# Performance work log

Measured on AMD Instinct MI355X. Metric: run time of the kernel, lower is better.

The kernel has to match this reference:

```python
import jax, jax.numpy as jnp
import numpy as np

N_USERS, N_ITEMS, D, B = 16384, 4096, 64, 2048
NAN_FRAC = 0.7
EPS = 1e-8


def setup_inputs() -> dict:
    key = jax.random.key(0)
    k1, k2, k3, k4, k5 = jax.random.split(key, 5)
    ratings = jax.random.uniform(k1, (N_USERS, N_ITEMS), jnp.float32, 1.0, 5.0)
    miss = jax.random.uniform(k2, (N_USERS, N_ITEMS)) < NAN_FRAC
    rating_matrix = jnp.where(miss, jnp.nan, ratings)
    user_embeddings = jax.random.normal(k3, (N_USERS, D), jnp.float32)
    user_indices = jax.random.randint(k4, (B,), 0, N_USERS)
    item_indices = jax.random.randint(k5, (B,), 0, N_ITEMS)
    return {
        "rating_matrix": rating_matrix,
        "user_embeddings": user_embeddings,
        "user_indices": user_indices,
        "item_indices": item_indices,
    }


def reference(rating_matrix, user_embeddings, user_indices, item_indices):
    n_users = rating_matrix.shape[0]

    # per-user average over non-NaN ratings (0.0 if user has no ratings)
    valid_r = ~jnp.isnan(rating_matrix)                      # [N, I]
    r0 = jnp.where(valid_r, rating_matrix, 0.0)
    cnt = valid_r.sum(axis=1)
    avg_ratings = jnp.where(cnt > 0, r0.sum(axis=1) / jnp.maximum(cnt, 1), 0.0)  # [N]

    u = user_embeddings[user_indices]                        # [B, d]
    # cosine similarity of each query user vs all users
    dots = jnp.einsum('bd,nd->bn', u, user_embeddings)       # [B, N]
    mag_u = jnp.linalg.norm(u, axis=1, keepdims=True)        # [B, 1]
    mag_v = jnp.linalg.norm(user_embeddings, axis=1)[None]   # [1, N]
    sim = dots / (mag_u * mag_v + EPS)                       # [B, N]

    # ratings of all users on each query item
    ratings_col = rating_matrix[:, item_indices].T           # [B, N]
    mask = ~jnp.isnan(ratings_col)                           # valid neighbor ratings
    mask = mask & (jnp.arange(n_users)[None, :] != user_indices[:, None])  # exclude self

    diff = jnp.where(mask, ratings_col - avg_ratings[None, :], 0.0)
    sim_m = jnp.where(mask, sim, 0.0)
    num = (diff * sim_m).sum(axis=1)                         # [B]
    den = jnp.abs(sim_m).sum(axis=1)                         # [B]
    den_safe = jnp.where(den == 0, 1.0, den)

    avg_u = avg_ratings[user_indices]
    return jnp.where(den == 0, avg_u, avg_u + num / den_safe)
```

## Files before the change

kernel.cpp:

```cpp
#include <hip/hip_runtime.h>
#include <math.h>

#define NU   16384
#define NI   4096
#define DDIM 64
#define BB   2048
#define GSTR8 2056

typedef unsigned short u16;
typedef unsigned char  u8;
typedef __attribute__((ext_vector_type(8))) short short8;
typedef __attribute__((ext_vector_type(4))) float f32x4;

static __device__ __forceinline__ u16 f2bf(float f) {
    union { float f; unsigned int u; } v; v.f = f;
    unsigned int u = v.u + 0x7FFFu + ((v.u >> 16) & 1u);
    return (u16)(u >> 16);
}

static __device__ __forceinline__ u8 enc_r(float r) {
    return (u8)__float2uint_rz(fmaf(r, 50.f, -48.5f));
}

__global__ __launch_bounds__(256) void k_qprep(
    const float* __restrict__ E, const int* __restrict__ uidx,
    u16* __restrict__ Ubf, int2* __restrict__ qinfo)
{
    const int lane = threadIdx.x & 63;
    const int b = blockIdx.x * 4 + (threadIdx.x >> 6);
    const int ub = uidx[b];
    const float e = E[(size_t)ub * DDIM + lane];
    float ss = e * e;
#pragma unroll
    for (int o = 32; o > 0; o >>= 1) ss += __shfl_xor(ss, o);
    Ubf[b * DDIM + lane] = f2bf(e);
    if (lane == 0) qinfo[b] = make_int2(ub, __float_as_int(rsqrtf(ss)));
}

__global__ __launch_bounds__(256) void k_fused(
    const float* __restrict__ R, const float* __restrict__ E,
    const int* __restrict__ iidx, const u16* __restrict__ Ubf,
    const int2* __restrict__ qinfo, float2* __restrict__ partials,
    float* __restrict__ avgAll)
{
    __shared__ u16 s_ii[BB];
    __shared__ u8  wrow[4][NI];
    __shared__ u8  g[16][GSTR8];
    __shared__ float sAvg[16], sInv[16];

    const int tid  = threadIdx.x;
    const int lane = tid & 63;
    const int wid  = tid >> 6;
    const int n0   = blockIdx.x * 16;

    for (int t = tid; t < BB; t += 256) s_ii[t] = (u16)iidx[t];

#pragma unroll
    for (int rs = 0; rs < 4; ++rs) {
        const int n = n0 + wid * 4 + rs;
        const float e = E[(size_t)n * DDIM + lane];
        float ss = e * e;
#pragma unroll
        for (int o = 32; o > 0; o >>= 1) ss += __shfl_xor(ss, o);
        if (lane == 0) sInv[wid * 4 + rs] = rsqrtf(ss);
    }
    __syncthreads();

#pragma unroll 1
    for (int rs = 0; rs < 4; ++rs) {
        const int rloc = wid * 4 + rs;
        const int n = n0 + rloc;
        const float4* R4 = (const float4*)(R + (size_t)n * NI);

        float4 v[16];
#pragma unroll
        for (int j = 0; j < 16; ++j) v[j] = R4[j * 64 + lane];

        float sum = 0.f;
        unsigned cnti = 0;
#pragma unroll
        for (int j = 0; j < 16; ++j) {
            const float4 x = v[j];
            sum += (x.x == x.x ? x.x : 0.f);
            sum += (x.y == x.y ? x.y : 0.f);
            sum += (x.z == x.z ? x.z : 0.f);
            sum += (x.w == x.w ? x.w : 0.f);
            cnti += (unsigned)__popcll(__ballot(x.x == x.x));
            cnti += (unsigned)__popcll(__ballot(x.y == x.y));
            cnti += (unsigned)__popcll(__ballot(x.z == x.z));
            cnti += (unsigned)__popcll(__ballot(x.w == x.w));
            uchar4 q;
            q.x = enc_r(x.x); q.y = enc_r(x.y); q.z = enc_r(x.z); q.w = enc_r(x.w);
            *(uchar4*)&wrow[wid][(j * 64 + lane) * 4] = q;
        }
#pragma unroll
        for (int o = 32; o > 0; o >>= 1) sum += __shfl_xor(sum, o);
        if (lane == 0) {
            const float C = (float)cnti;
            const float a = (C > 0.f) ? (sum / C) : 0.f;
            sAvg[rloc] = a;
            avgAll[n] = a;
        }
        asm volatile("s_waitcnt lgkmcnt(0)" ::: "memory");

#pragma unroll
        for (int t = 0; t < 8; ++t) {
            const int b4 = (t * 64 + lane) * 4;
            const ushort4 ii = *(const ushort4*)&s_ii[b4];
            uchar4 q;
            q.x = wrow[wid][ii.x];
            q.y = wrow[wid][ii.y];
            q.z = wrow[wid][ii.z];
            q.w = wrow[wid][ii.w];
            *(uchar4*)&g[rloc][b4] = q;
        }
    }
    __syncthreads();

    const int lo = lane & 15;
    const int hi = lane >> 4;

    short8 a[2];
#pragma unroll
    for (int kg = 0; kg < 2; ++kg) {
        const float* ep = E + (size_t)(n0 + lo) * DDIM + kg * 32 + hi * 8;
        const float4 e0 = *(const float4*)(ep);
        const float4 e1 = *(const float4*)(ep + 4);
        union { short8 v; u16 u[8]; } t;
        t.u[0] = f2bf(e0.x); t.u[1] = f2bf(e0.y); t.u[2] = f2bf(e0.z); t.u[3] = f2bf(e0.w);
        t.u[4] = f2bf(e1.x); t.u[5] = f2bf(e1.y); t.u[6] = f2bf(e1.z); t.u[7] = f2bf(e1.w);
        a[kg] = t.v;
    }
    float avr[4], ivr[4];
#pragma unroll
    for (int r = 0; r < 4; ++r) { avr[r] = sAvg[hi * 4 + r]; ivr[r] = sInv[hi * 4 + r]; }

    float2* pout = partials + (size_t)blockIdx.x * BB;

#pragma unroll 1
    for (int j = 0; j < 32; ++j) {
        const int b0 = (j * 4 + wid) * 16;
        const int2 q = qinfo[b0 + lo];
        const float inv_mu = __int_as_float(q.y);

        const short8 bf0 = *(const short8*)(Ubf + (size_t)(b0 + lo) * DDIM + hi * 8);
        const short8 bf1 = *(const short8*)(Ubf + (size_t)(b0 + lo) * DDIM + 32 + hi * 8);

        f32x4 c = {0.f, 0.f, 0.f, 0.f};
        c = __builtin_amdgcn_mfma_f32_16x16x32_bf16(a[0], bf0, c, 0, 0, 0);
        c = __builtin_amdgcn_mfma_f32_16x16x32_bf16(a[1], bf1, c, 0, 0, 0);

        float fnum = 0.f, fden = 0.f;
#pragma unroll
        for (int r = 0; r < 4; ++r) {
            const int nr = n0 + hi * 4 + r;
            const u8 qg = g[hi * 4 + r][b0 + lo];
            const bool valid = (qg != 0) && (nr != q.x);
            const float gv = (float)(int)qg * 0.02f + 0.98f;
            const float s  = valid ? c[r] * (inv_mu * ivr[r]) : 0.f;
            fnum += (gv - avr[r]) * s;
            fden += fabsf(s);
        }
        fnum += __shfl_xor(fnum, 16); fden += __shfl_xor(fden, 16);
        fnum += __shfl_xor(fnum, 32); fden += __shfl_xor(fden, 32);
        if (lane < 16) pout[b0 + lane] = make_float2(fnum, fden);
    }
}

__global__ __launch_bounds__(256) void k_final(
    const float2* __restrict__ partials, const int2* __restrict__ qinfo,
    const float* __restrict__ avgAll, float* __restrict__ out)
{
    __shared__ float sn[8][32], sd[8][32];
    const int tid = threadIdx.x;
    const int bl  = tid & 31;
    const int ch  = tid >> 5;
    const int b   = blockIdx.x * 32 + bl;
    float n = 0.f, d = 0.f;
    for (int blk = ch; blk < NU / 16; blk += 8) {
        const float2 p = partials[(size_t)blk * BB + b];
        n += p.x; d += p.y;
    }
    sn[ch][bl] = n; sd[ch][bl] = d;
    __syncthreads();
    if (tid < 32) {
        float N = 0.f, D = 0.f;
#pragma unroll
        for (int c2 = 0; c2 < 8; ++c2) { N += sn[c2][tid]; D += sd[c2][tid]; }
        const int bb = blockIdx.x * 32 + tid;
        const float au = avgAll[qinfo[bb].x];
        out[bb] = (D == 0.f) ? au : (au + N / D);
    }
}

extern "C" void kernel_launch(void* const* d_in, const int* in_sizes, int n_in,
                              void* d_out, int out_size, void* d_ws, size_t ws_size,
                              hipStream_t stream)
{
    const float* R    = (const float*)d_in[0];
    const float* E    = (const float*)d_in[1];
    const int*   uidx = (const int*)d_in[2];
    const int*   iidx = (const int*)d_in[3];
    float* out = (float*)d_out;

    char* p = (char*)d_ws;
    float2* parts  = (float2*)p;  p += (size_t)(NU / 16) * BB * 8;
    u16*    Ubf    = (u16*)p;     p += (size_t)BB * DDIM * 2;
    int2*   qinfo  = (int2*)p;    p += (size_t)BB * 8;
    float*  avgAll = (float*)p;   p += (size_t)NU * 4;

    k_qprep<<<BB / 4, 256, 0, stream>>>(E, uidx, Ubf, qinfo);
    k_fused<<<NU / 16, 256, 0, stream>>>(R, E, iidx, Ubf, qinfo, parts, avgAll);
    k_final<<<BB / 32, 256, 0, stream>>>(parts, qinfo, avgAll, out);
}
```

Measured before the change: 457.3 us.

## Split fused kernel into streaming gather kernel and MFMA accumulate kernel

```diff
diff --git a/kernel.cpp b/kernel.cpp
--- a/kernel.cpp
+++ b/kernel.cpp
@@ -5,7 +5,6 @@
 #define NI   4096
 #define DDIM 64
 #define BB   2048
-#define GSTR8 2056
 
 typedef unsigned short u16;
 typedef unsigned char  u8;
@@ -37,72 +36,63 @@
     if (lane == 0) qinfo[b] = make_int2(ub, __float_as_int(rsqrtf(ss)));
 }
 
-__global__ __launch_bounds__(256) void k_fused(
+__global__ __launch_bounds__(256, 8) void k_stream(
     const float* __restrict__ R, const float* __restrict__ E,
-    const int* __restrict__ iidx, const u16* __restrict__ Ubf,
-    const int2* __restrict__ qinfo, float2* __restrict__ partials,
-    float* __restrict__ avgAll)
+    const int* __restrict__ iidx,
+    float2* __restrict__ avgInv, u8* __restrict__ Gq)
 {
     __shared__ u16 s_ii[BB];
     __shared__ u8  wrow[4][NI];
-    __shared__ u8  g[16][GSTR8];
-    __shared__ float sAvg[16], sInv[16];
-
     const int tid  = threadIdx.x;
     const int lane = tid & 63;
     const int wid  = tid >> 6;
-    const int n0   = blockIdx.x * 16;
 
     for (int t = tid; t < BB; t += 256) s_ii[t] = (u16)iidx[t];
-
-#pragma unroll
-    for (int rs = 0; rs < 4; ++rs) {
-        const int n = n0 + wid * 4 + rs;
+    __syncthreads();
+
+    const int wg = blockIdx.x * 4 + wid;
+#pragma unroll 1
+    for (int rr = 0; rr < 2; ++rr) {
+        const int n = wg * 2 + rr;
+        const float4* R4 = (const float4*)(R + (size_t)n * NI);
         const float e = E[(size_t)n * DDIM + lane];
-        float ss = e * e;
-#pragma unroll
-        for (int o = 32; o > 0; o >>= 1) ss += __shfl_xor(ss, o);
-        if (lane == 0) sInv[wid * 4 + rs] = rsqrtf(ss);
-    }
-    __syncthreads();
-
-#pragma unroll 1
-    for (int rs = 0; rs < 4; ++rs) {
-        const int rloc = wid * 4 + rs;
-        const int n = n0 + rloc;
-        const float4* R4 = (const float4*)(R + (size_t)n * NI);
-
-        float4 v[16];
-#pragma unroll
-        for (int j = 0; j < 16; ++j) v[j] = R4[j * 64 + lane];
 
         float sum = 0.f;
         unsigned cnti = 0;
-#pragma unroll
-        for (int j = 0; j < 16; ++j) {
-            const float4 x = v[j];
-            sum += (x.x == x.x ? x.x : 0.f);
-            sum += (x.y == x.y ? x.y : 0.f);
-            sum += (x.z == x.z ? x.z : 0.f);
-            sum += (x.w == x.w ? x.w : 0.f);
-            cnti += (unsigned)__popcll(__ballot(x.x == x.x));
-            cnti += (unsigned)__popcll(__ballot(x.y == x.y));
-            cnti += (unsigned)__popcll(__ballot(x.z == x.z));
-            cnti += (unsigned)__popcll(__ballot(x.w == x.w));
-            uchar4 q;
-            q.x = enc_r(x.x); q.y = enc_r(x.y); q.z = enc_r(x.z); q.w = enc_r(x.w);
-            *(uchar4*)&wrow[wid][(j * 64 + lane) * 4] = q;
-        }
-#pragma unroll
-        for (int o = 32; o > 0; o >>= 1) sum += __shfl_xor(sum, o);
+#pragma unroll 1
+        for (int h = 0; h < 2; ++h) {
+            float4 v[8];
+#pragma unroll
+            for (int j = 0; j < 8; ++j) v[j] = R4[(h * 8 + j) * 64 + lane];
+#pragma unroll
+            for (int j = 0; j < 8; ++j) {
+                const float4 x = v[j];
+                sum += (x.x == x.x ? x.x : 0.f);
+                sum += (x.y == x.y ? x.y : 0.f);
+                sum += (x.z == x.z ? x.z : 0.f);
+                sum += (x.w == x.w ? x.w : 0.f);
+                cnti += (unsigned)__popcll(__ballot(x.x == x.x));
+                cnti += (unsigned)__popcll(__ballot(x.y == x.y));
+                cnti += (unsigned)__popcll(__ballot(x.z == x.z));
+                cnti += (unsigned)__popcll(__ballot(x.w == x.w));
+                uchar4 q;
+                q.x = enc_r(x.x); q.y = enc_r(x.y); q.z = enc_r(x.z); q.w = enc_r(x.w);
+                *(uchar4*)&wrow[wid][((h * 8 + j) * 64 + lane) * 4] = q;
+            }
+        }
+        float ss = e * e;
+#pragma unroll
+        for (int o = 32; o > 0; o >>= 1) {
+            ss  += __shfl_xor(ss, o);
+            sum += __shfl_xor(sum, o);
+        }
         if (lane == 0) {
             const float C = (float)cnti;
-            const float a = (C > 0.f) ? (sum / C) : 0.f;
-            sAvg[rloc] = a;
-            avgAll[n] = a;
+            avgInv[n] = make_float2((C > 0.f) ? (sum / C) : 0.f, rsqrtf(ss));
         }
         asm volatile("s_waitcnt lgkmcnt(0)" ::: "memory");
 
+        u8* Gn = Gq + (size_t)n * BB;
 #pragma unroll
         for (int t = 0; t < 8; ++t) {
             const int b4 = (t * 64 + lane) * 4;
@@ -112,13 +102,22 @@
             q.y = wrow[wid][ii.y];
             q.z = wrow[wid][ii.z];
             q.w = wrow[wid][ii.w];
-            *(uchar4*)&g[rloc][b4] = q;
-        }
-    }
-    __syncthreads();
-
-    const int lo = lane & 15;
-    const int hi = lane >> 4;
+            *(uchar4*)&Gn[b4] = q;
+        }
+    }
+}
+
+__global__ __launch_bounds__(256) void k_accum(
+    const float* __restrict__ E, const u16* __restrict__ Ubf,
+    const u8* __restrict__ Gq, const float2* __restrict__ avgInv,
+    const int2* __restrict__ qinfo, float2* __restrict__ partials)
+{
+    const int tid  = threadIdx.x;
+    const int lane = tid & 63;
+    const int wid  = tid >> 6;
+    const int lo   = lane & 15;
+    const int hi   = lane >> 4;
+    const int n0   = blockIdx.x * 16;
 
     short8 a[2];
 #pragma unroll
@@ -133,7 +132,10 @@
     }
     float avr[4], ivr[4];
 #pragma unroll
-    for (int r = 0; r < 4; ++r) { avr[r] = sAvg[hi * 4 + r]; ivr[r] = sInv[hi * 4 + r]; }
+    for (int r = 0; r < 4; ++r) {
+        const float2 ai = avgInv[n0 + hi * 4 + r];
+        avr[r] = ai.x; ivr[r] = ai.y;
+    }
 
     float2* pout = partials + (size_t)blockIdx.x * BB;
 
@@ -154,7 +156,7 @@
 #pragma unroll
         for (int r = 0; r < 4; ++r) {
             const int nr = n0 + hi * 4 + r;
-            const u8 qg = g[hi * 4 + r][b0 + lo];
+            const u8 qg = Gq[(size_t)nr * BB + b0 + lo];
             const bool valid = (qg != 0) && (nr != q.x);
             const float gv = (float)(int)qg * 0.02f + 0.98f;
             const float s  = valid ? c[r] * (inv_mu * ivr[r]) : 0.f;
@@ -169,7 +171,7 @@
 
 __global__ __launch_bounds__(256) void k_final(
     const float2* __restrict__ partials, const int2* __restrict__ qinfo,
-    const float* __restrict__ avgAll, float* __restrict__ out)
+    const float2* __restrict__ avgInv, float* __restrict__ out)
 {
     __shared__ float sn[8][32], sd[8][32];
     const int tid = threadIdx.x;
@@ -188,7 +190,7 @@
 #pragma unroll
         for (int c2 = 0; c2 < 8; ++c2) { N += sn[c2][tid]; D += sd[c2][tid]; }
         const int bb = blockIdx.x * 32 + tid;
-        const float au = avgAll[qinfo[bb].x];
+        const float au = avgInv[qinfo[bb].x].x;
         out[bb] = (D == 0.f) ? au : (au + N / D);
     }
 }
@@ -205,11 +207,13 @@
 
     char* p = (char*)d_ws;
     float2* parts  = (float2*)p;  p += (size_t)(NU / 16) * BB * 8;
+    u8*     Gq     = (u8*)p;      p += (size_t)NU * BB;
     u16*    Ubf    = (u16*)p;     p += (size_t)BB * DDIM * 2;
     int2*   qinfo  = (int2*)p;    p += (size_t)BB * 8;
-    float*  avgAll = (float*)p;   p += (size_t)NU * 4;
+    float2* avgInv = (float2*)p;  p += (size_t)NU * 8;
 
     k_qprep<<<BB / 4, 256, 0, stream>>>(E, uidx, Ubf, qinfo);
-    k_fused<<<NU / 16, 256, 0, stream>>>(R, E, iidx, Ubf, qinfo, parts, avgAll);
-    k_final<<<BB / 32, 256, 0, stream>>>(parts, qinfo, avgAll, out);
-}
+    k_stream<<<NU / 8, 256, 0, stream>>>(R, E, iidx, avgInv, Gq);
+    k_accum<<<NU / 16, 256, 0, stream>>>(E, Ubf, Gq, avgInv, qinfo, parts);
+    k_final<<<BB / 32, 256, 0, stream>>>(parts, qinfo, avgInv, out);
+}
```

New measurement: 444.2 us. -2.9%, faster.

## Split fused kernel into row-sum, norm, and gather-accumulate kernels

Applied to the files above, without the earlier changes.

```diff
diff --git a/kernel.cpp b/kernel.cpp
--- a/kernel.cpp
+++ b/kernel.cpp
@@ -37,88 +37,89 @@
     if (lane == 0) qinfo[b] = make_int2(ub, __float_as_int(rsqrtf(ss)));
 }
 
-__global__ __launch_bounds__(256) void k_fused(
+__global__ __launch_bounds__(256) void k_sums(
+    const float* __restrict__ R, float* __restrict__ rowsum, float* __restrict__ rowcnt)
+{
+    const int lane = threadIdx.x & 63;
+    const int row  = blockIdx.x;
+    const int qtr  = threadIdx.x >> 6;
+    const float4* R4 = (const float4*)(R + (size_t)row * NI) + qtr * 256;
+
+    const float4 a = R4[lane];
+    const float4 b = R4[lane + 64];
+    const float4 c = R4[lane + 128];
+    const float4 d = R4[lane + 192];
+
+    float s = 0.f, cn = 0.f;
+#define ACC(v) do { \
+    if ((v).x == (v).x) { s += (v).x; cn += 1.f; } \
+    if ((v).y == (v).y) { s += (v).y; cn += 1.f; } \
+    if ((v).z == (v).z) { s += (v).z; cn += 1.f; } \
+    if ((v).w == (v).w) { s += (v).w; cn += 1.f; } } while (0)
+    ACC(a); ACC(b); ACC(c); ACC(d);
+#undef ACC
+#pragma unroll
+    for (int o = 32; o > 0; o >>= 1) {
+        s  += __shfl_xor(s, o);
+        cn += __shfl_xor(cn, o);
+    }
+    if (lane == 0) {
+        atomicAdd(&rowsum[row], s);
+        atomicAdd(&rowcnt[row], cn);
+    }
+}
+
+__global__ __launch_bounds__(256) void k_enorm(
+    const float* __restrict__ E, float* __restrict__ normInv)
+{
+    const int lane = threadIdx.x & 63;
+    const int n = blockIdx.x * 4 + (threadIdx.x >> 6);
+    const float e = E[(size_t)n * DDIM + lane];
+    float ss = e * e;
+#pragma unroll
+    for (int o = 32; o > 0; o >>= 1) ss += __shfl_xor(ss, o);
+    if (lane == 0) normInv[n] = rsqrtf(ss);
+}
+
+__global__ __launch_bounds__(256) void k_accum(
     const float* __restrict__ R, const float* __restrict__ E,
     const int* __restrict__ iidx, const u16* __restrict__ Ubf,
-    const int2* __restrict__ qinfo, float2* __restrict__ partials,
-    float* __restrict__ avgAll)
-{
-    __shared__ u16 s_ii[BB];
-    __shared__ u8  wrow[4][NI];
-    __shared__ u8  g[16][GSTR8];
-    __shared__ float sAvg[16], sInv[16];
+    const int2* __restrict__ qinfo,
+    const float* __restrict__ rowsum, const float* __restrict__ rowcnt,
+    const float* __restrict__ normInv, float2* __restrict__ partials)
+{
+    __shared__ u8 g[16][GSTR8];
 
     const int tid  = threadIdx.x;
     const int lane = tid & 63;
     const int wid  = tid >> 6;
+    const int lo   = lane & 15;
+    const int hi   = lane >> 4;
     const int n0   = blockIdx.x * 16;
 
-    for (int t = tid; t < BB; t += 256) s_ii[t] = (u16)iidx[t];
-
-#pragma unroll
-    for (int rs = 0; rs < 4; ++rs) {
-        const int n = n0 + wid * 4 + rs;
-        const float e = E[(size_t)n * DDIM + lane];
-        float ss = e * e;
-#pragma unroll
-        for (int o = 32; o > 0; o >>= 1) ss += __shfl_xor(ss, o);
-        if (lane == 0) sInv[wid * 4 + rs] = rsqrtf(ss);
-    }
-    __syncthreads();
-
-#pragma unroll 1
-    for (int rs = 0; rs < 4; ++rs) {
-        const int rloc = wid * 4 + rs;
-        const int n = n0 + rloc;
-        const float4* R4 = (const float4*)(R + (size_t)n * NI);
-
-        float4 v[16];
-#pragma unroll
-        for (int j = 0; j < 16; ++j) v[j] = R4[j * 64 + lane];
-
-        float sum = 0.f;
-        unsigned cnti = 0;
-#pragma unroll
-        for (int j = 0; j < 16; ++j) {
-            const float4 x = v[j];
-            sum += (x.x == x.x ? x.x : 0.f);
-            sum += (x.y == x.y ? x.y : 0.f);
-            sum += (x.z == x.z ? x.z : 0.f);
-            sum += (x.w == x.w ? x.w : 0.f);
-            cnti += (unsigned)__popcll(__ballot(x.x == x.x));
-            cnti += (unsigned)__popcll(__ballot(x.y == x.y));
-            cnti += (unsigned)__popcll(__ballot(x.z == x.z));
-            cnti += (unsigned)__popcll(__ballot(x.w == x.w));
-            uchar4 q;
-            q.x = enc_r(x.x); q.y = enc_r(x.y); q.z = enc_r(x.z); q.w = enc_r(x.w);
-            *(uchar4*)&wrow[wid][(j * 64 + lane) * 4] = q;
-        }
-#pragma unroll
-        for (int o = 32; o > 0; o >>= 1) sum += __shfl_xor(sum, o);
-        if (lane == 0) {
-            const float C = (float)cnti;
-            const float a = (C > 0.f) ? (sum / C) : 0.f;
-            sAvg[rloc] = a;
-            avgAll[n] = a;
-        }
-        asm volatile("s_waitcnt lgkmcnt(0)" ::: "memory");
-
-#pragma unroll
-        for (int t = 0; t < 8; ++t) {
-            const int b4 = (t * 64 + lane) * 4;
-            const ushort4 ii = *(const ushort4*)&s_ii[b4];
-            uchar4 q;
-            q.x = wrow[wid][ii.x];
-            q.y = wrow[wid][ii.y];
-            q.z = wrow[wid][ii.z];
-            q.w = wrow[wid][ii.w];
-            *(uchar4*)&g[rloc][b4] = q;
-        }
-    }
-    __syncthreads();
-
-    const int lo = lane & 15;
-    const int hi = lane >> 4;
+    const int4 ii0 = ((const int4*)iidx)[tid];
+    const int4 ii1 = ((const int4*)iidx)[tid + 256];
+
+#pragma unroll 2
+    for (int rloc = 0; rloc < 16; ++rloc) {
+        const float* Rn = R + (size_t)(n0 + rloc) * NI;
+        const float a0 = Rn[ii0.x], a1 = Rn[ii0.y], a2 = Rn[ii0.z], a3 = Rn[ii0.w];
+        const float b0 = Rn[ii1.x], b1 = Rn[ii1.y], b2 = Rn[ii1.z], b3 = Rn[ii1.w];
+        uchar4 qa, qb;
+        qa.x = enc_r(a0); qa.y = enc_r(a1); qa.z = enc_r(a2); qa.w = enc_r(a3);
+        qb.x = enc_r(b0); qb.y = enc_r(b1); qb.z = enc_r(b2); qb.w = enc_r(b3);
+        *(uchar4*)&g[rloc][tid * 4]         = qa;
+        *(uchar4*)&g[rloc][(tid + 256) * 4] = qb;
+    }
+
+    float avr[4], ivr[4];
+#pragma unroll
+    for (int r = 0; r < 4; ++r) {
+        const int nr = n0 + hi * 4 + r;
+        const float cn = rowcnt[nr];
+        avr[r] = (cn > 0.f) ? (rowsum[nr] / cn) : 0.f;
+        ivr[r] = normInv[nr];
+    }
 
     short8 a[2];
 #pragma unroll
@@ -131,9 +132,8 @@
         t.u[4] = f2bf(e1.x); t.u[5] = f2bf(e1.y); t.u[6] = f2bf(e1.z); t.u[7] = f2bf(e1.w);
         a[kg] = t.v;
     }
-    float avr[4], ivr[4];
-#pragma unroll
-    for (int r = 0; r < 4; ++r) { avr[r] = sAvg[hi * 4 + r]; ivr[r] = sInv[hi * 4 + r]; }
+
+    __syncthreads();
 
     float2* pout = partials + (size_t)blockIdx.x * BB;
 
@@ -169,7 +169,8 @@
 
 __global__ __launch_bounds__(256) void k_final(
     const float2* __restrict__ partials, const int2* __restrict__ qinfo,
-    const float* __restrict__ avgAll, float* __restrict__ out)
+    const float* __restrict__ rowsum, const float* __restrict__ rowcnt,
+    float* __restrict__ out)
 {
     __shared__ float sn[8][32], sd[8][32];
     const int tid = threadIdx.x;
@@ -188,7 +189,9 @@
 #pragma unroll
         for (int c2 = 0; c2 < 8; ++c2) { N += sn[c2][tid]; D += sd[c2][tid]; }
         const int bb = blockIdx.x * 32 + tid;
-        const float au = avgAll[qinfo[bb].x];
+        const int ub = qinfo[bb].x;
+        const float cn = rowcnt[ub];
+        const float au = (cn > 0.f) ? (rowsum[ub] / cn) : 0.f;
         out[bb] = (D == 0.f) ? au : (au + N / D);
     }
 }
@@ -204,12 +207,18 @@
     float* out = (float*)d_out;
 
     char* p = (char*)d_ws;
-    float2* parts  = (float2*)p;  p += (size_t)(NU / 16) * BB * 8;
-    u16*    Ubf    = (u16*)p;     p += (size_t)BB * DDIM * 2;
-    int2*   qinfo  = (int2*)p;    p += (size_t)BB * 8;
-    float*  avgAll = (float*)p;   p += (size_t)NU * 4;
+    float2* parts   = (float2*)p;  p += (size_t)(NU / 16) * BB * 8;
+    u16*    Ubf     = (u16*)p;     p += (size_t)BB * DDIM * 2;
+    int2*   qinfo   = (int2*)p;    p += (size_t)BB * 8;
+    float*  rowsum  = (float*)p;   p += (size_t)NU * 4;
+    float*  rowcnt  = (float*)p;   p += (size_t)NU * 4;
+    float*  normInv = (float*)p;   p += (size_t)NU * 4;
+
+    hipMemsetAsync(rowsum, 0, (size_t)NU * 2 * sizeof(float), stream);
 
     k_qprep<<<BB / 4, 256, 0, stream>>>(E, uidx, Ubf, qinfo);
-    k_fused<<<NU / 16, 256, 0, stream>>>(R, E, iidx, Ubf, qinfo, parts, avgAll);
-    k_final<<<BB / 32, 256, 0, stream>>>(parts, qinfo, avgAll, out);
-}
+    k_sums<<<NU, 256, 0, stream>>>(R, rowsum, rowcnt);
+    k_enorm<<<NU / 4, 256, 0, stream>>>(E, normInv);
+    k_accum<<<NU / 16, 256, 0, stream>>>(R, E, iidx, Ubf, qinfo, rowsum, rowcnt, normInv, parts);
+    k_final<<<BB / 32, 256, 0, stream>>>(parts, qinfo, rowsum, rowcnt, out);
+}
```

Measured after the change: 521.3 us. 1.14x slower.
